# Kernel tuning notes

Hardware: AMD Instinct MI355X
Metric: run time of the kernel (lower is better)

## Reference

```python
import jax, jax.numpy as jnp
import numpy as np

C = 256
CLS_DIM = 512
GROUPS = C // 4
EPS = 1e-5


def group_norm(x, w, b, groups=GROUPS, eps=EPS):
    # x: [N, C, H, W]
    N, Cc, H, W = x.shape
    xg = x.reshape(N, groups, Cc // groups, H, W)
    mu = xg.mean(axis=(2, 3, 4), keepdims=True)
    var = xg.var(axis=(2, 3, 4), keepdims=True)
    xn = ((xg - mu) * jax.lax.rsqrt(var + eps)).reshape(N, Cc, H, W)
    return xn * w[None, :, None, None] + b[None, :, None, None]


def setup_inputs() -> dict:
    key = jax.random.key(0)
    ks = jax.random.split(key, 12)
    N, H, W = 32, 64, 64
    s = 0.02
    return {
        "X": jax.random.normal(ks[0], (N, C, H, W), jnp.float32),
        "cls": jax.random.normal(ks[1], (N, CLS_DIM), jnp.float32),
        "ln_w": 1.0 + s * jax.random.normal(ks[2], (C,), jnp.float32),
        "ln_b": s * jax.random.normal(ks[3], (C,), jnp.float32),
        "wq": jax.random.normal(ks[4], (C, CLS_DIM), jnp.float32) / np.sqrt(CLS_DIM),
        "bq": s * jax.random.normal(ks[5], (C,), jnp.float32),
        "wk": jax.random.normal(ks[6], (C, CLS_DIM), jnp.float32) / np.sqrt(CLS_DIM),
        "bk": s * jax.random.normal(ks[7], (C,), jnp.float32),
        "conv_w": jax.random.normal(ks[8], (C, C), jnp.float32) / np.sqrt(C),
        "conv_b": s * jax.random.normal(ks[9], (C,), jnp.float32),
        "gn_w": 1.0 + s * jax.random.normal(ks[10], (C,), jnp.float32),
        "gn_b": s * jax.random.normal(ks[11], (C,), jnp.float32),
    }


def reference(X, cls, ln_w, ln_b, wq, bq, wk, bk, conv_w, conv_b, gn_w, gn_b):
    res = X
    Xn = group_norm(X, ln_w, ln_b)
    # NOTE: original code swaps names: K <- Q_emb(cls), Q <- K_emb(cls)
    K = jax.nn.elu(cls @ wq.T + bq) + 1.0              # [N, C]
    Q = (jax.nn.elu(cls @ wk.T + bk) + 1.0) / jnp.sqrt(jnp.float32(C))
    # einsum 'nclw,nco->nolw' with o=1: per-pixel channel contraction with K
    s = jnp.einsum("nchw,nc->nhw", Xn, K)              # [N, H, W]
    # einsum 'nolw,nco->nclw': rank-1 outer product with Q
    X2 = s[:, None, :, :] * Q[:, :, None, None]        # [N, C, H, W]
    # 1x1 conv
    Y = jnp.einsum("nchw,oc->nohw", X2, conv_w) + conv_b[None, :, None, None]
    return group_norm(Y, gn_w, gn_b) + res
```

## Files before the change

### kernel.cpp

```cpp
#include <hip/hip_runtime.h>
#include <math.h>

#define EPSV 1e-5f

typedef float f4v __attribute__((ext_vector_type(4)));

__device__ __forceinline__ float waveReduceSum(float v) {
#pragma unroll
    for (int o = 32; o > 0; o >>= 1) v += __shfl_down(v, o, 64);
    return v;
}

__global__ void k_kq(const float* __restrict__ cls,
                     const float* __restrict__ wq, const float* __restrict__ bq,
                     const float* __restrict__ wk, const float* __restrict__ bk,
                     const float* __restrict__ ln_w,
                     float* __restrict__ Kb, float* __restrict__ Qb,
                     float* __restrict__ Kw) {
    int w = blockIdx.x * 4 + (threadIdx.x >> 6);
    int lane = threadIdx.x & 63;
    int n = w >> 8, c = w & 255;
    const float* cp = cls + (size_t)n * 512;
    const float* qp = wq + (size_t)c * 512;
    const float* kp = wk + (size_t)c * 512;
    float aK = 0.f, aQ = 0.f;
#pragma unroll
    for (int i = 0; i < 8; ++i) {
        int kk = lane + i * 64;
        float cv = cp[kk];
        aK += cv * qp[kk];
        aQ += cv * kp[kk];
    }
    aK = waveReduceSum(aK);
    aQ = waveReduceSum(aQ);
    if (lane == 0) {
        float xk = aK + bq[c];
        float xq = aQ + bk[c];
        float Kv = (xk > 0.f ? xk : expf(xk) - 1.f) + 1.f;
        float Qv = ((xq > 0.f ? xq : expf(xq) - 1.f) + 1.f) * 0.0625f;
        Kb[w] = Kv;
        Qb[w] = Qv;
        Kw[w] = Kv * ln_w[c];
    }
}

__global__ void __launch_bounds__(512) k_pass1(
        const float* __restrict__ X, const float* __restrict__ Kw,
        float* __restrict__ W, float* __restrict__ Sp, float* __restrict__ S2p) {
    int n = blockIdx.x >> 4, tile = blockIdx.x & 15;
    int wv = threadIdx.x >> 6, lane = threadIdx.x & 63;
    __shared__ float kws[256];
    if (threadIdx.x < 256) kws[threadIdx.x] = Kw[n * 256 + threadIdx.x];
    __syncthreads();
    int pix = tile * 256 + lane * 4;
    const float* xb = X + ((size_t)n * 256 << 12) + pix;
#pragma unroll
    for (int go = 0; go < 8; ++go) {
        int g = wv * 8 + go;
        int c0 = g * 4;
        float ax = 0.f, ay = 0.f, az = 0.f, aw = 0.f;
        float s = 0.f, s2 = 0.f;
#pragma unroll
        for (int j = 0; j < 4; ++j) {
            float4 v = *(const float4*)(xb + ((size_t)(c0 + j) << 12));
            float kv = kws[c0 + j];
            ax += kv * v.x; ay += kv * v.y; az += kv * v.z; aw += kv * v.w;
            s  += v.x + v.y + v.z + v.w;
            s2 += v.x * v.x + v.y * v.y + v.z * v.z + v.w * v.w;
        }
        float4 acc = {ax, ay, az, aw};
        *(float4*)(W + ((size_t)(n * 64 + g) << 12) + pix) = acc;
        s = waveReduceSum(s);
        s2 = waveReduceSum(s2);
        if (lane == 0) {
            Sp[blockIdx.x * 64 + g] = s;
            S2p[blockIdx.x * 64 + g] = s2;
        }
    }
}

__global__ void k_prep2(const float* __restrict__ Sp, const float* __restrict__ S2p,
                        const float* __restrict__ Kb, const float* __restrict__ Qb,
                        const float* __restrict__ ln_w, const float* __restrict__ ln_b,
                        const float* __restrict__ conv_w,
                        float* __restrict__ inv1, float* __restrict__ B,
                        float* __restrict__ R) {
    int n = blockIdx.x, t = threadIdx.x;
    __shared__ float ivs[64], mus[64], qs[256], red[4];
    qs[t] = Qb[n * 256 + t];
    if (t < 64) {
        float S = 0.f, S2 = 0.f;
#pragma unroll
        for (int tl = 0; tl < 16; ++tl) {
            S  += Sp[(n * 16 + tl) * 64 + t];
            S2 += S2p[(n * 16 + tl) * 64 + t];
        }
        float mu = S * (1.f / 16384.f);
        float var = S2 * (1.f / 16384.f) - mu * mu;
        float iv = rsqrtf(var + EPSV);
        mus[t] = mu; ivs[t] = iv;
        inv1[n * 64 + t] = iv;
    }
    __syncthreads();
    float Kv = Kb[n * 256 + t];
    float termB = Kv * (ln_b[t] - ln_w[t] * ivs[t >> 2] * mus[t >> 2]);
    int lane = t & 63, wid = t >> 6;
    float r = waveReduceSum(termB);
    if (lane == 0) red[wid] = r;
    __syncthreads();
    if (t == 0) B[n] = red[0] + red[1] + red[2] + red[3];
    float acc = 0.f;
    const float* cw = conv_w + (size_t)t * 256;
#pragma unroll 4
    for (int c2 = 0; c2 < 256; ++c2) acc += cw[c2] * qs[c2];
    R[n * 256 + t] = acc;
}

__global__ void k_pass3(const float* __restrict__ W, const float* __restrict__ inv1,
                        const float* __restrict__ B, float* __restrict__ sbuf,
                        float* __restrict__ p1, float* __restrict__ p2) {
    int n = blockIdx.x >> 2, tile = blockIdx.x & 3;
    int t = threadIdx.x;
    __shared__ float ivs[64];
    __shared__ float q1[4], q2[4];
    if (t < 64) ivs[t] = inv1[n * 64 + t];
    __syncthreads();
    int pix = tile * 1024 + t * 4;
    const float* wb = W + ((size_t)n * 64 << 12) + pix;
    float Bn = B[n];
    float sx = Bn, sy = Bn, sz = Bn, sw = Bn;
#pragma unroll 8
    for (int g = 0; g < 64; ++g) {
        float4 v = *(const float4*)(wb + ((size_t)g << 12));
        float iv = ivs[g];
        sx += iv * v.x; sy += iv * v.y; sz += iv * v.z; sw += iv * v.w;
    }
    float4 s4 = {sx, sy, sz, sw};
    *(float4*)(sbuf + n * 4096 + pix) = s4;
    float r1 = sx + sy + sz + sw;
    float r2 = sx * sx + sy * sy + sz * sz + sw * sw;
    r1 = waveReduceSum(r1);
    r2 = waveReduceSum(r2);
    int lane = t & 63, wid = t >> 6;
    if (lane == 0) { q1[wid] = r1; q2[wid] = r2; }
    __syncthreads();
    if (t == 0) {
        p1[blockIdx.x] = q1[0] + q1[1] + q1[2] + q1[3];
        p2[blockIdx.x] = q2[0] + q2[1] + q2[2] + q2[3];
    }
}

__global__ void k_ab(const float* __restrict__ p1, const float* __restrict__ p2,
                     const float* __restrict__ R, const float* __restrict__ conv_b,
                     const float* __restrict__ gn_w, const float* __restrict__ gn_b,
                     float* __restrict__ alpha, float* __restrict__ beta) {
    int n = blockIdx.x, t = threadIdx.x;
    __shared__ float Ms1s, Ms2s;
    if (t == 0) {
        float a = 0.f, b = 0.f;
#pragma unroll
        for (int i = 0; i < 4; ++i) { a += p1[n * 4 + i]; b += p2[n * 4 + i]; }
        Ms1s = a * (1.f / 4096.f);
        Ms2s = b * (1.f / 4096.f);
    }
    __syncthreads();
    float Ms1 = Ms1s, Ms2 = Ms2s;
    int g = t >> 2;
    float mR = 0.f, mR2 = 0.f, mRb = 0.f, mb = 0.f, mb2 = 0.f;
#pragma unroll
    for (int j = 0; j < 4; ++j) {
        float r = R[n * 256 + g * 4 + j];
        float b = conv_b[g * 4 + j];
        mR += r; mR2 += r * r; mRb += r * b; mb += b; mb2 += b * b;
    }
    mR *= 0.25f; mR2 *= 0.25f; mRb *= 0.25f; mb *= 0.25f; mb2 *= 0.25f;
    float mu = Ms1 * mR + mb;
    float var = Ms2 * mR2 + 2.f * Ms1 * mRb + mb2 - mu * mu;
    float iv = rsqrtf(var + EPSV);
    float r = R[n * 256 + t];
    alpha[n * 256 + t] = r * iv * gn_w[t];
    beta[n * 256 + t] = (conv_b[t] - mu) * iv * gn_w[t] + gn_b[t];
}

__global__ void k_final(const float* __restrict__ X, const float* __restrict__ sbuf,
                        const float* __restrict__ alpha, const float* __restrict__ beta,
                        float* __restrict__ out) {
    size_t idx4 = (size_t)blockIdx.x * 256 + threadIdx.x;
    size_t e = idx4 * 4;
    int n = (int)(e >> 20);
    int rem = (int)(e & 1048575);
    int o = rem >> 12;
    int pix = rem & 4095;
    float4 x = ((const float4*)X)[idx4];
    float4 s = *(const float4*)(sbuf + n * 4096 + pix);
    float a = alpha[n * 256 + o], b = beta[n * 256 + o];
    f4v r;
    r.x = fmaf(s.x, a, b) + x.x;
    r.y = fmaf(s.y, a, b) + x.y;
    r.z = fmaf(s.z, a, b) + x.z;
    r.w = fmaf(s.w, a, b) + x.w;
    __builtin_nontemporal_store(r, (f4v*)out + idx4);
}

extern "C" void kernel_launch(void* const* d_in, const int* in_sizes, int n_in,
                              void* d_out, int out_size, void* d_ws, size_t ws_size,
                              hipStream_t stream) {
    const float* X      = (const float*)d_in[0];
    const float* cls    = (const float*)d_in[1];
    const float* ln_w   = (const float*)d_in[2];
    const float* ln_b   = (const float*)d_in[3];
    const float* wq     = (const float*)d_in[4];
    const float* bq     = (const float*)d_in[5];
    const float* wk     = (const float*)d_in[6];
    const float* bk     = (const float*)d_in[7];
    const float* conv_w = (const float*)d_in[8];
    const float* conv_b = (const float*)d_in[9];
    const float* gn_w   = (const float*)d_in[10];
    const float* gn_b   = (const float*)d_in[11];

    float* ws = (float*)d_ws;
    float* Kb    = ws;
    float* Qb    = ws + 8192;
    float* Kw    = ws + 16384;
    float* Sp    = ws + 24576;
    float* S2p   = ws + 57344;
    float* inv1  = ws + 90112;
    float* B     = ws + 92160;
    float* R     = ws + 92192;
    float* p1    = ws + 100384;
    float* p2    = ws + 100512;
    float* alpha = ws + 100640;
    float* beta  = ws + 108832;
    float* sbuf  = ws + 131072;
    float* W     = ws + 262144;

    k_kq<<<2048, 256, 0, stream>>>(cls, wq, bq, wk, bk, ln_w, Kb, Qb, Kw);
    k_pass1<<<512, 512, 0, stream>>>(X, Kw, W, Sp, S2p);
    k_prep2<<<32, 256, 0, stream>>>(Sp, S2p, Kb, Qb, ln_w, ln_b, conv_w, inv1, B, R);
    k_pass3<<<128, 256, 0, stream>>>(W, inv1, B, sbuf, p1, p2);
    k_ab<<<32, 256, 0, stream>>>(p1, p2, R, conv_b, gn_w, gn_b, alpha, beta);
    k_final<<<32768, 256, 0, stream>>>(X, sbuf, alpha, beta, (float*)d_out);
}
```

Baseline: 94.98 us.

## Fuse small per-sample kernels into head, stats and final passes

Cuts the launch chain from six kernels to four. The K/Q projections, the Kw scaling and the conv_w·Q product move into a single per-sample head kernel, and the first GroupNorm bias term is split algebraically into T1 and T2 so it can be finished inside the s-computation kernel. The alpha/beta computation is folded into the final elementwise kernel, which now handles one (n,o) plane per block. This removes launch gaps and intermediate buffers, but the head kernel runs only 32 blocks, each serially reading the full wq and wk matrices, and every final block recomputes the group statistics.

```diff
diff --git a/kernel.cpp b/kernel.cpp
--- a/kernel.cpp
+++ b/kernel.cpp
@@ -11,36 +11,62 @@
     return v;
 }
 
-__global__ void k_kq(const float* __restrict__ cls,
-                     const float* __restrict__ wq, const float* __restrict__ bq,
-                     const float* __restrict__ wk, const float* __restrict__ bk,
-                     const float* __restrict__ ln_w,
-                     float* __restrict__ Kb, float* __restrict__ Qb,
-                     float* __restrict__ Kw) {
-    int w = blockIdx.x * 4 + (threadIdx.x >> 6);
-    int lane = threadIdx.x & 63;
-    int n = w >> 8, c = w & 255;
-    const float* cp = cls + (size_t)n * 512;
-    const float* qp = wq + (size_t)c * 512;
-    const float* kp = wk + (size_t)c * 512;
-    float aK = 0.f, aQ = 0.f;
-#pragma unroll
-    for (int i = 0; i < 8; ++i) {
-        int kk = lane + i * 64;
-        float cv = cp[kk];
-        aK += cv * qp[kk];
-        aQ += cv * kp[kk];
-    }
-    aK = waveReduceSum(aK);
-    aQ = waveReduceSum(aQ);
-    if (lane == 0) {
-        float xk = aK + bq[c];
-        float xq = aQ + bk[c];
+__global__ void __launch_bounds__(512) k_head(
+        const float* __restrict__ cls,
+        const float* __restrict__ wq, const float* __restrict__ bq,
+        const float* __restrict__ wk, const float* __restrict__ bk,
+        const float* __restrict__ ln_w, const float* __restrict__ ln_b,
+        const float* __restrict__ conv_w,
+        float* __restrict__ Kw, float* __restrict__ T1,
+        float* __restrict__ T2, float* __restrict__ R) {
+    int n = blockIdx.x, t = threadIdx.x;
+    __shared__ float clsS[512];
+    __shared__ float qs[256];
+    __shared__ float kwS[256];
+    __shared__ float red[4];
+    clsS[t] = cls[(size_t)n * 512 + t];
+    __syncthreads();
+    const float4* cp4 = (const float4*)clsS;
+    if (t < 256) {
+        const float4* wr = (const float4*)(wq + (size_t)t * 512);
+        float acc = 0.f;
+#pragma unroll 8
+        for (int k = 0; k < 128; ++k) {
+            float4 w4 = wr[k], c4 = cp4[k];
+            acc += w4.x * c4.x + w4.y * c4.y + w4.z * c4.z + w4.w * c4.w;
+        }
+        float xk = acc + bq[t];
         float Kv = (xk > 0.f ? xk : expf(xk) - 1.f) + 1.f;
-        float Qv = ((xq > 0.f ? xq : expf(xq) - 1.f) + 1.f) * 0.0625f;
-        Kb[w] = Kv;
-        Qb[w] = Qv;
-        Kw[w] = Kv * ln_w[c];
+        float kw = Kv * ln_w[t];
+        Kw[n * 256 + t] = kw;
+        kwS[t] = kw;
+        float r = waveReduceSum(Kv * ln_b[t]);
+        if ((t & 63) == 0) red[t >> 6] = r;
+    } else {
+        int c = t - 256;
+        const float4* wr = (const float4*)(wk + (size_t)c * 512);
+        float acc = 0.f;
+#pragma unroll 8
+        for (int k = 0; k < 128; ++k) {
+            float4 w4 = wr[k], c4 = cp4[k];
+            acc += w4.x * c4.x + w4.y * c4.y + w4.z * c4.z + w4.w * c4.w;
+        }
+        float xq = acc + bk[c];
+        qs[c] = ((xq > 0.f ? xq : expf(xq) - 1.f) + 1.f) * 0.0625f;
+    }
+    __syncthreads();
+    if (t == 0) T1[n] = red[0] + red[1] + red[2] + red[3];
+    if (t < 64) T2[n * 64 + t] = kwS[4 * t] + kwS[4 * t + 1] + kwS[4 * t + 2] + kwS[4 * t + 3];
+    if (t < 256) {
+        const float4* cw = (const float4*)(conv_w + (size_t)t * 256);
+        const float4* q4 = (const float4*)qs;
+        float acc = 0.f;
+#pragma unroll 8
+        for (int k = 0; k < 64; ++k) {
+            float4 w4 = cw[k], v4 = q4[k];
+            acc += w4.x * v4.x + w4.y * v4.y + w4.z * v4.z + w4.w * v4.w;
+        }
+        R[n * 256 + t] = acc;
     }
 }
 
@@ -79,15 +105,16 @@
     }
 }
 
-__global__ void k_prep2(const float* __restrict__ Sp, const float* __restrict__ S2p,
-                        const float* __restrict__ Kb, const float* __restrict__ Qb,
-                        const float* __restrict__ ln_w, const float* __restrict__ ln_b,
-                        const float* __restrict__ conv_w,
-                        float* __restrict__ inv1, float* __restrict__ B,
-                        float* __restrict__ R) {
-    int n = blockIdx.x, t = threadIdx.x;
-    __shared__ float ivs[64], mus[64], qs[256], red[4];
-    qs[t] = Qb[n * 256 + t];
+__global__ void k_s(const float* __restrict__ W,
+                    const float* __restrict__ Sp, const float* __restrict__ S2p,
+                    const float* __restrict__ T1, const float* __restrict__ T2,
+                    float* __restrict__ sbuf,
+                    float* __restrict__ p1, float* __restrict__ p2) {
+    int n = blockIdx.x >> 2, tile = blockIdx.x & 3;
+    int t = threadIdx.x;
+    __shared__ float ivs[64];
+    __shared__ float Bsh;
+    __shared__ float q1[4], q2[4];
     if (t < 64) {
         float S = 0.f, S2 = 0.f;
 #pragma unroll
@@ -98,36 +125,14 @@
         float mu = S * (1.f / 16384.f);
         float var = S2 * (1.f / 16384.f) - mu * mu;
         float iv = rsqrtf(var + EPSV);
-        mus[t] = mu; ivs[t] = iv;
-        inv1[n * 64 + t] = iv;
-    }
-    __syncthreads();
-    float Kv = Kb[n * 256 + t];
-    float termB = Kv * (ln_b[t] - ln_w[t] * ivs[t >> 2] * mus[t >> 2]);
-    int lane = t & 63, wid = t >> 6;
-    float r = waveReduceSum(termB);
-    if (lane == 0) red[wid] = r;
-    __syncthreads();
-    if (t == 0) B[n] = red[0] + red[1] + red[2] + red[3];
-    float acc = 0.f;
-    const float* cw = conv_w + (size_t)t * 256;
-#pragma unroll 4
-    for (int c2 = 0; c2 < 256; ++c2) acc += cw[c2] * qs[c2];
-    R[n * 256 + t] = acc;
-}
-
-__global__ void k_pass3(const float* __restrict__ W, const float* __restrict__ inv1,
-                        const float* __restrict__ B, float* __restrict__ sbuf,
-                        float* __restrict__ p1, float* __restrict__ p2) {
-    int n = blockIdx.x >> 2, tile = blockIdx.x & 3;
-    int t = threadIdx.x;
-    __shared__ float ivs[64];
-    __shared__ float q1[4], q2[4];
-    if (t < 64) ivs[t] = inv1[n * 64 + t];
+        ivs[t] = iv;
+        float r = waveReduceSum(iv * mu * T2[n * 64 + t]);
+        if (t == 0) Bsh = T1[n] - r;
+    }
     __syncthreads();
     int pix = tile * 1024 + t * 4;
     const float* wb = W + ((size_t)n * 64 << 12) + pix;
-    float Bn = B[n];
+    float Bn = Bsh;
     float sx = Bn, sy = Bn, sz = Bn, sw = Bn;
 #pragma unroll 8
     for (int g = 0; g < 64; ++g) {
@@ -137,10 +142,8 @@
     }
     float4 s4 = {sx, sy, sz, sw};
     *(float4*)(sbuf + n * 4096 + pix) = s4;
-    float r1 = sx + sy + sz + sw;
-    float r2 = sx * sx + sy * sy + sz * sz + sw * sw;
-    r1 = waveReduceSum(r1);
-    r2 = waveReduceSum(r2);
+    float r1 = waveReduceSum(sx + sy + sz + sw);
+    float r2 = waveReduceSum(sx * sx + sy * sy + sz * sz + sw * sw);
     int lane = t & 63, wid = t >> 6;
     if (lane == 0) { q1[wid] = r1; q2[wid] = r2; }
     __syncthreads();
@@ -150,56 +153,49 @@
     }
 }
 
-__global__ void k_ab(const float* __restrict__ p1, const float* __restrict__ p2,
-                     const float* __restrict__ R, const float* __restrict__ conv_b,
-                     const float* __restrict__ gn_w, const float* __restrict__ gn_b,
-                     float* __restrict__ alpha, float* __restrict__ beta) {
-    int n = blockIdx.x, t = threadIdx.x;
-    __shared__ float Ms1s, Ms2s;
-    if (t == 0) {
-        float a = 0.f, b = 0.f;
-#pragma unroll
-        for (int i = 0; i < 4; ++i) { a += p1[n * 4 + i]; b += p2[n * 4 + i]; }
-        Ms1s = a * (1.f / 4096.f);
-        Ms2s = b * (1.f / 4096.f);
-    }
-    __syncthreads();
-    float Ms1 = Ms1s, Ms2 = Ms2s;
-    int g = t >> 2;
+__global__ void k_final(const float* __restrict__ X, const float* __restrict__ sbuf,
+                        const float* __restrict__ p1, const float* __restrict__ p2,
+                        const float* __restrict__ R, const float* __restrict__ conv_b,
+                        const float* __restrict__ gn_w, const float* __restrict__ gn_b,
+                        float* __restrict__ out) {
+    int b = blockIdx.x;
+    int n = b >> 8, o = b & 255;
+    int t = threadIdx.x;
+    float a1 = 0.f, a2 = 0.f;
+#pragma unroll
+    for (int i = 0; i < 4; ++i) { a1 += p1[n * 4 + i]; a2 += p2[n * 4 + i]; }
+    float Ms1 = a1 * (1.f / 4096.f);
+    float Ms2 = a2 * (1.f / 4096.f);
+    int g = o >> 2;
     float mR = 0.f, mR2 = 0.f, mRb = 0.f, mb = 0.f, mb2 = 0.f;
 #pragma unroll
     for (int j = 0; j < 4; ++j) {
         float r = R[n * 256 + g * 4 + j];
-        float b = conv_b[g * 4 + j];
-        mR += r; mR2 += r * r; mRb += r * b; mb += b; mb2 += b * b;
+        float bb = conv_b[g * 4 + j];
+        mR += r; mR2 += r * r; mRb += r * bb; mb += bb; mb2 += bb * bb;
     }
     mR *= 0.25f; mR2 *= 0.25f; mRb *= 0.25f; mb *= 0.25f; mb2 *= 0.25f;
     float mu = Ms1 * mR + mb;
     float var = Ms2 * mR2 + 2.f * Ms1 * mRb + mb2 - mu * mu;
     float iv = rsqrtf(var + EPSV);
-    float r = R[n * 256 + t];
-    alpha[n * 256 + t] = r * iv * gn_w[t];
-    beta[n * 256 + t] = (conv_b[t] - mu) * iv * gn_w[t] + gn_b[t];
-}
-
-__global__ void k_final(const float* __restrict__ X, const float* __restrict__ sbuf,
-                        const float* __restrict__ alpha, const float* __restrict__ beta,
-                        float* __restrict__ out) {
-    size_t idx4 = (size_t)blockIdx.x * 256 + threadIdx.x;
-    size_t e = idx4 * 4;
-    int n = (int)(e >> 20);
-    int rem = (int)(e & 1048575);
-    int o = rem >> 12;
-    int pix = rem & 4095;
-    float4 x = ((const float4*)X)[idx4];
-    float4 s = *(const float4*)(sbuf + n * 4096 + pix);
-    float a = alpha[n * 256 + o], b = beta[n * 256 + o];
-    f4v r;
-    r.x = fmaf(s.x, a, b) + x.x;
-    r.y = fmaf(s.y, a, b) + x.y;
-    r.z = fmaf(s.z, a, b) + x.z;
-    r.w = fmaf(s.w, a, b) + x.w;
-    __builtin_nontemporal_store(r, (f4v*)out + idx4);
+    float alpha = R[n * 256 + o] * iv * gn_w[o];
+    float beta = (conv_b[o] - mu) * iv * gn_w[o] + gn_b[o];
+
+    const float4* xp = (const float4*)X + (size_t)b * 1024;
+    const float4* sp = (const float4*)sbuf + (size_t)n * 1024;
+    f4v* op = (f4v*)out + (size_t)b * 1024;
+#pragma unroll
+    for (int i = 0; i < 4; ++i) {
+        int idx = i * 256 + t;
+        float4 x = xp[idx];
+        float4 s = sp[idx];
+        f4v r;
+        r.x = fmaf(s.x, alpha, beta) + x.x;
+        r.y = fmaf(s.y, alpha, beta) + x.y;
+        r.z = fmaf(s.z, alpha, beta) + x.z;
+        r.w = fmaf(s.w, alpha, beta) + x.w;
+        __builtin_nontemporal_store(r, op + idx);
+    }
 }
 
 extern "C" void kernel_launch(void* const* d_in, const int* in_sizes, int n_in,
@@ -219,25 +215,21 @@
     const float* gn_b   = (const float*)d_in[11];
 
     float* ws = (float*)d_ws;
-    float* Kb    = ws;
-    float* Qb    = ws + 8192;
-    float* Kw    = ws + 16384;
-    float* Sp    = ws + 24576;
-    float* S2p   = ws + 57344;
-    float* inv1  = ws + 90112;
-    float* B     = ws + 92160;
-    float* R     = ws + 92192;
-    float* p1    = ws + 100384;
-    float* p2    = ws + 100512;
-    float* alpha = ws + 100640;
-    float* beta  = ws + 108832;
-    float* sbuf  = ws + 131072;
-    float* W     = ws + 262144;
-
-    k_kq<<<2048, 256, 0, stream>>>(cls, wq, bq, wk, bk, ln_w, Kb, Qb, Kw);
+    float* Kw   = ws;
+    float* T1   = ws + 8192;
+    float* T2   = ws + 8256;
+    float* R    = ws + 10304;
+    float* Sp   = ws + 18496;
+    float* S2p  = ws + 51264;
+    float* p1   = ws + 84032;
+    float* p2   = ws + 84160;
+    float* sbuf = ws + 131072;
+    float* W    = ws + 262144;
+
+    k_head<<<32, 512, 0, stream>>>(cls, wq, bq, wk, bk, ln_w, ln_b, conv_w,
+                                   Kw, T1, T2, R);
     k_pass1<<<512, 512, 0, stream>>>(X, Kw, W, Sp, S2p);
-    k_prep2<<<32, 256, 0, stream>>>(Sp, S2p, Kb, Qb, ln_w, ln_b, conv_w, inv1, B, R);
-    k_pass3<<<128, 256, 0, stream>>>(W, inv1, B, sbuf, p1, p2);
-    k_ab<<<32, 256, 0, stream>>>(p1, p2, R, conv_b, gn_w, gn_b, alpha, beta);
-    k_final<<<32768, 256, 0, stream>>>(X, sbuf, alpha, beta, (float*)d_out);
-}
+    k_s<<<128, 256, 0, stream>>>(W, Sp, S2p, T1, T2, sbuf, p1, p2);
+    k_final<<<8192, 256, 0, stream>>>(X, sbuf, p1, p2, R, conv_b, gn_w, gn_b,
+                                      (float*)d_out);
+}
```

After: 115.7 us. 21.8% more time.
